# Kernel optimization log

Hardware: AMD Instinct MI355X
Metric: run time of the kernel (lower is better)

The kernel has to match this reference:

```python
import math
import jax, jax.numpy as jnp
import numpy as np

CT = {"SDD": 1000.0, "SCD": 500.0, "det_interval": 1.0, "num_det": 736}


def ramp_filter_np(ct, scale):
    # Standard equiangular fan-beam ramp filter (utility.ramp_filter):
    #   h[0] = 1/(8*db^2); h[n odd] = -1/(2*(pi*sin(n*db))^2); h[n even!=0] = 0
    db = ct["det_interval"] / ct["SDD"] * scale  # angular detector pitch at this scale
    n_det = int(ct["num_det"] // scale)
    n = np.arange(-(n_det - 1), n_det)  # length K = 2*n_det - 1
    h = np.zeros(n.shape, dtype=np.float32)
    h[n == 0] = 1.0 / (8.0 * db ** 2)
    odd = (n % 2) != 0
    h[odd] = -0.5 / (np.pi * np.sin(n[odd] * db)) ** 2
    return h


def setup_inputs() -> dict:
    key = jax.random.key(0)
    scale = 1
    batch, ch, view, det = 16, 1, 1152, CT["num_det"] // scale
    sinogram = jax.random.normal(key, (batch, ch, view, det), dtype=jnp.float32)
    delta_b = CT["det_interval"] / CT["SDD"]
    # recon_filter = ramp_filter * scale * delta_b, shaped [1,1,1,K] (OIHW)
    filt = ramp_filter_np(CT, scale) * scale * delta_b
    recon_filter = jnp.asarray(filt, dtype=jnp.float32)[None, None, None, :]
    return {"sinogram": sinogram, "recon_filter": recon_filter, "scale": scale}


def reference(sinogram, recon_filter, scale):
    det = sinogram.shape[-1]
    # cosine fan-beam pre-weighting
    s_range = (CT["det_interval"]
               * jnp.linspace((1.0 - det) / 2.0, (det - 1.0) / 2.0, det, dtype=jnp.float32)
               * scale) / CT["SDD"]
    cos_weight = (CT["SCD"] / 10000.0) * jnp.cos(s_range)  # [det]
    x = sinogram * cos_weight[None, None, None, :]
    # 1D ramp-filter convolution along detector axis (F.conv2d with 1xK kernel)
    K = recon_filter.shape[-1]
    pad = K // 2
    out = jax.lax.conv_general_dilated(
        x, recon_filter,
        window_strides=(1, 1),
        padding=[(0, 0), (pad, pad)],
        dimension_numbers=("NCHW", "OIHW", "NCHW"),
    )
    return out
```

## Files before the change

kernel.cpp:

```cpp
#include <hip/hip_runtime.h>
#include <stdint.h>

typedef unsigned short ushort_t;
typedef ushort_t u16x8 __attribute__((ext_vector_type(8)));
typedef __bf16 bf16x8 __attribute__((ext_vector_type(8)));
typedef float f32x4 __attribute__((ext_vector_type(4)));

#define DET 736
#define NPAD 768

#define GPTR(p) ((const __attribute__((address_space(1))) unsigned int*)(p))
#define LPTR(p) ((__attribute__((address_space(3))) unsigned int*)(p))

__device__ __forceinline__ ushort_t f2bf(float f) {
    unsigned u = __builtin_bit_cast(unsigned, f);
    u += 0x7FFFu + ((u >> 16) & 1u);
    return (ushort_t)(u >> 16);
}

__global__ void cast_x(const float* __restrict__ in, ushort_t* __restrict__ out, int total) {
    int idx = (blockIdx.x * blockDim.x + threadIdx.x) * 8;
    if (idx >= total) return;
    float4 a = *(const float4*)(in + idx);
    float4 b = *(const float4*)(in + idx + 4);
    u16x8 o;
    o[0] = f2bf(a.x); o[1] = f2bf(a.y); o[2] = f2bf(a.z); o[3] = f2bf(a.w);
    o[4] = f2bf(b.x); o[5] = f2bf(b.y); o[6] = f2bf(b.z); o[7] = f2bf(b.w);
    *(u16x8*)(out + idx) = o;
}

__global__ void prep_bt(const float* __restrict__ filt, ushort_t* __restrict__ Bt) {
    int idx = blockIdx.x * blockDim.x + threadIdx.x;
    if (idx >= NPAD * DET) return;
    int n = idx / DET;
    int k = idx - n * DET;
    float w = 0.05f * cosf(((float)k - 367.5f) * 0.001f);
    float v = (n < DET) ? w * filt[k - n + (DET - 1)] : 0.0f;
    Bt[idx] = f2bf(v);
}

__global__ __launch_bounds__(256) void gemm_bt(
    const ushort_t* __restrict__ A,
    const ushort_t* __restrict__ Bt,
    float* __restrict__ C, int M)
{
    __shared__ ushort_t As[128 * 32];
    __shared__ ushort_t Bs[128 * 32];

    const int tid  = threadIdx.x;
    const int lane = tid & 63;
    const int warp = tid >> 6;
    const int wm   = warp & 1;
    const int wn   = warp >> 1;
    const int quad = lane >> 4;
    const int l16  = lane & 15;

    const size_t row_a0 = (size_t)blockIdx.x * 128;
    const size_t row_b0 = (size_t)blockIdx.y * 128;

    const int c0 = warp * 64 + lane;
    const int c1 = c0 + 256;
    const int r0 = c0 >> 2, q0 = c0 & 3;
    const int r1 = c1 >> 2, q1 = c1 & 3;

    const ushort_t* a0p = A  + (row_a0 + r0) * DET + q0 * 8;
    const ushort_t* a1p = A  + (row_a0 + r1) * DET + q1 * 8;
    const ushort_t* b0p = Bt + (row_b0 + r0) * DET + q0 * 8;
    const ushort_t* b1p = Bt + (row_b0 + r1) * DET + q1 * 8;

    f32x4 acc[4][4];
#pragma unroll
    for (int i = 0; i < 4; ++i)
#pragma unroll
        for (int jx = 0; jx < 4; ++jx)
            acc[i][jx] = (f32x4){0.f, 0.f, 0.f, 0.f};

    for (int k0 = 0; k0 < DET; k0 += 32) {
        if (k0) __syncthreads();
        __builtin_amdgcn_global_load_lds(GPTR(a0p + k0), LPTR(As + warp * 512),        16, 0, 0);
        __builtin_amdgcn_global_load_lds(GPTR(a1p + k0), LPTR(As + 2048 + warp * 512), 16, 0, 0);
        __builtin_amdgcn_global_load_lds(GPTR(b0p + k0), LPTR(Bs + warp * 512),        16, 0, 0);
        __builtin_amdgcn_global_load_lds(GPTR(b1p + k0), LPTR(Bs + 2048 + warp * 512), 16, 0, 0);
        __syncthreads();

        u16x8 af[4], bfr[4];
#pragma unroll
        for (int mi = 0; mi < 4; ++mi)
            af[mi] = *(const u16x8*)(As + (wm * 64 + mi * 16 + l16) * 32 + quad * 8);
#pragma unroll
        for (int ni = 0; ni < 4; ++ni)
            bfr[ni] = *(const u16x8*)(Bs + (wn * 64 + ni * 16 + l16) * 32 + quad * 8);
#pragma unroll
        for (int mi = 0; mi < 4; ++mi)
#pragma unroll
            for (int ni = 0; ni < 4; ++ni)
                acc[mi][ni] = __builtin_amdgcn_mfma_f32_16x16x32_bf16(
                    __builtin_bit_cast(bf16x8, af[mi]),
                    __builtin_bit_cast(bf16x8, bfr[ni]),
                    acc[mi][ni], 0, 0, 0);
    }

#pragma unroll
    for (int mi = 0; mi < 4; ++mi) {
#pragma unroll
        for (int ni = 0; ni < 4; ++ni) {
            int colg = (int)row_b0 + wn * 64 + ni * 16 + l16;
            if (colg < DET) {
#pragma unroll
                for (int r = 0; r < 4; ++r) {
                    size_t rowg = row_a0 + wm * 64 + mi * 16 + quad * 4 + r;
                    C[rowg * DET + colg] = acc[mi][ni][r];
                }
            }
        }
    }
}

extern "C" void kernel_launch(void* const* d_in, const int* in_sizes, int n_in,
                              void* d_out, int out_size, void* d_ws, size_t ws_size,
                              hipStream_t stream) {
    const float* sino = (const float*)d_in[0];
    const float* filt = (const float*)d_in[1];
    int total = in_sizes[0];
    int M = total / DET;

    ushort_t* Xbf = (ushort_t*)d_ws;
    ushort_t* Btb = Xbf + (size_t)total;
    float* out = (float*)d_out;

    cast_x<<<(total / 8 + 255) / 256, 256, 0, stream>>>(sino, Xbf, total);
    prep_bt<<<(NPAD * DET + 255) / 256, 256, 0, stream>>>(filt, Btb);

    dim3 grid(M / 128, NPAD / 128);
    gemm_bt<<<grid, 256, 0, stream>>>(Xbf, Btb, out, M);
}
```

Measured before the change: 144.0 us.

## Fuse fp32-to-bf16 cast into GEMM with register-prefetched double-buffered LDS

Removes the separate cast kernel and its bf16 intermediate buffer. The GEMM now reads fp32 sinogram rows directly and converts them to bf16 in registers before storing to LDS. The main loop is double-buffered: the next K tile is loaded into registers while MFMAs run on the current tile, and LDS rows are padded to stride 40 to reduce bank conflicts. In exchange, the A tile is read from global memory as fp32 by every N-block, which doubles A read bytes per block. It also gives up the direct global-to-LDS load path and uses more registers.

New measurement: 148.9 us. 1.03x slower.

```diff
diff --git a/kernel.cpp b/kernel.cpp
--- a/kernel.cpp
+++ b/kernel.cpp
@@ -1,5 +1,4 @@
 #include <hip/hip_runtime.h>
-#include <stdint.h>
 
 typedef unsigned short ushort_t;
 typedef ushort_t u16x8 __attribute__((ext_vector_type(8)));
@@ -8,25 +7,13 @@
 
 #define DET 736
 #define NPAD 768
-
-#define GPTR(p) ((const __attribute__((address_space(1))) unsigned int*)(p))
-#define LPTR(p) ((__attribute__((address_space(3))) unsigned int*)(p))
+#define NITER 23
+#define LDSTR 40
 
 __device__ __forceinline__ ushort_t f2bf(float f) {
     unsigned u = __builtin_bit_cast(unsigned, f);
     u += 0x7FFFu + ((u >> 16) & 1u);
     return (ushort_t)(u >> 16);
-}
-
-__global__ void cast_x(const float* __restrict__ in, ushort_t* __restrict__ out, int total) {
-    int idx = (blockIdx.x * blockDim.x + threadIdx.x) * 8;
-    if (idx >= total) return;
-    float4 a = *(const float4*)(in + idx);
-    float4 b = *(const float4*)(in + idx + 4);
-    u16x8 o;
-    o[0] = f2bf(a.x); o[1] = f2bf(a.y); o[2] = f2bf(a.z); o[3] = f2bf(a.w);
-    o[4] = f2bf(b.x); o[5] = f2bf(b.y); o[6] = f2bf(b.z); o[7] = f2bf(b.w);
-    *(u16x8*)(out + idx) = o;
 }
 
 __global__ void prep_bt(const float* __restrict__ filt, ushort_t* __restrict__ Bt) {
@@ -39,13 +26,13 @@
     Bt[idx] = f2bf(v);
 }
 
-__global__ __launch_bounds__(256) void gemm_bt(
-    const ushort_t* __restrict__ A,
+__global__ __launch_bounds__(256) void gemm_fused(
+    const float* __restrict__ A,
     const ushort_t* __restrict__ Bt,
     float* __restrict__ C, int M)
 {
-    __shared__ ushort_t As[128 * 32];
-    __shared__ ushort_t Bs[128 * 32];
+    __shared__ ushort_t As[2][128 * LDSTR];
+    __shared__ ushort_t Bs[2][128 * LDSTR];
 
     const int tid  = threadIdx.x;
     const int lane = tid & 63;
@@ -58,15 +45,11 @@
     const size_t row_a0 = (size_t)blockIdx.x * 128;
     const size_t row_b0 = (size_t)blockIdx.y * 128;
 
-    const int c0 = warp * 64 + lane;
-    const int c1 = c0 + 256;
-    const int r0 = c0 >> 2, q0 = c0 & 3;
-    const int r1 = c1 >> 2, q1 = c1 & 3;
-
-    const ushort_t* a0p = A  + (row_a0 + r0) * DET + q0 * 8;
-    const ushort_t* a1p = A  + (row_a0 + r1) * DET + q1 * 8;
-    const ushort_t* b0p = Bt + (row_b0 + r0) * DET + q0 * 8;
-    const ushort_t* b1p = Bt + (row_b0 + r1) * DET + q1 * 8;
+    const int srow = tid >> 1;
+    const int sh   = (tid & 1) * 16;
+    const float*    ap = A  + (row_a0 + srow) * DET + sh;
+    const ushort_t* bp = Bt + (row_b0 + srow) * DET + sh;
+    const int soff = srow * LDSTR + sh;
 
     f32x4 acc[4][4];
 #pragma unroll
@@ -75,21 +58,48 @@
         for (int jx = 0; jx < 4; ++jx)
             acc[i][jx] = (f32x4){0.f, 0.f, 0.f, 0.f};
 
-    for (int k0 = 0; k0 < DET; k0 += 32) {
-        if (k0) __syncthreads();
-        __builtin_amdgcn_global_load_lds(GPTR(a0p + k0), LPTR(As + warp * 512),        16, 0, 0);
-        __builtin_amdgcn_global_load_lds(GPTR(a1p + k0), LPTR(As + 2048 + warp * 512), 16, 0, 0);
-        __builtin_amdgcn_global_load_lds(GPTR(b0p + k0), LPTR(Bs + warp * 512),        16, 0, 0);
-        __builtin_amdgcn_global_load_lds(GPTR(b1p + k0), LPTR(Bs + 2048 + warp * 512), 16, 0, 0);
-        __syncthreads();
+    {
+        f32x4 a0 = *(const f32x4*)(ap + 0);
+        f32x4 a1 = *(const f32x4*)(ap + 4);
+        f32x4 a2 = *(const f32x4*)(ap + 8);
+        f32x4 a3 = *(const f32x4*)(ap + 12);
+        u16x8 b0 = *(const u16x8*)(bp + 0);
+        u16x8 b1 = *(const u16x8*)(bp + 8);
+        bf16x8 c0 = {(__bf16)a0[0], (__bf16)a0[1], (__bf16)a0[2], (__bf16)a0[3],
+                     (__bf16)a1[0], (__bf16)a1[1], (__bf16)a1[2], (__bf16)a1[3]};
+        bf16x8 c1 = {(__bf16)a2[0], (__bf16)a2[1], (__bf16)a2[2], (__bf16)a2[3],
+                     (__bf16)a3[0], (__bf16)a3[1], (__bf16)a3[2], (__bf16)a3[3]};
+        *(u16x8*)(&As[0][soff])     = __builtin_bit_cast(u16x8, c0);
+        *(u16x8*)(&As[0][soff + 8]) = __builtin_bit_cast(u16x8, c1);
+        *(u16x8*)(&Bs[0][soff])     = b0;
+        *(u16x8*)(&Bs[0][soff + 8]) = b1;
+    }
+    __syncthreads();
+
+    for (int it = 0; it < NITER; ++it) {
+        const int cur = it & 1;
+        const int nxt = cur ^ 1;
+        const int k1 = (it + 1) * 32;
+        const bool pf = (it + 1 < NITER);
+
+        f32x4 a0, a1, a2, a3; u16x8 b0, b1;
+        if (pf) {
+            a0 = *(const f32x4*)(ap + k1);
+            a1 = *(const f32x4*)(ap + k1 + 4);
+            a2 = *(const f32x4*)(ap + k1 + 8);
+            a3 = *(const f32x4*)(ap + k1 + 12);
+            b0 = *(const u16x8*)(bp + k1);
+            b1 = *(const u16x8*)(bp + k1 + 8);
+        }
 
         u16x8 af[4], bfr[4];
 #pragma unroll
         for (int mi = 0; mi < 4; ++mi)
-            af[mi] = *(const u16x8*)(As + (wm * 64 + mi * 16 + l16) * 32 + quad * 8);
+            af[mi] = *(const u16x8*)(&As[cur][(wm * 64 + mi * 16 + l16) * LDSTR + quad * 8]);
 #pragma unroll
         for (int ni = 0; ni < 4; ++ni)
-            bfr[ni] = *(const u16x8*)(Bs + (wn * 64 + ni * 16 + l16) * 32 + quad * 8);
+            bfr[ni] = *(const u16x8*)(&Bs[cur][(wn * 64 + ni * 16 + l16) * LDSTR + quad * 8]);
+
 #pragma unroll
         for (int mi = 0; mi < 4; ++mi)
 #pragma unroll
@@ -98,6 +108,18 @@
                     __builtin_bit_cast(bf16x8, af[mi]),
                     __builtin_bit_cast(bf16x8, bfr[ni]),
                     acc[mi][ni], 0, 0, 0);
+
+        if (pf) {
+            bf16x8 c0 = {(__bf16)a0[0], (__bf16)a0[1], (__bf16)a0[2], (__bf16)a0[3],
+                         (__bf16)a1[0], (__bf16)a1[1], (__bf16)a1[2], (__bf16)a1[3]};
+            bf16x8 c1 = {(__bf16)a2[0], (__bf16)a2[1], (__bf16)a2[2], (__bf16)a2[3],
+                         (__bf16)a3[0], (__bf16)a3[1], (__bf16)a3[2], (__bf16)a3[3]};
+            *(u16x8*)(&As[nxt][soff])     = __builtin_bit_cast(u16x8, c0);
+            *(u16x8*)(&As[nxt][soff + 8]) = __builtin_bit_cast(u16x8, c1);
+            *(u16x8*)(&Bs[nxt][soff])     = b0;
+            *(u16x8*)(&Bs[nxt][soff + 8]) = b1;
+        }
+        __syncthreads();
     }
 
 #pragma unroll
@@ -124,13 +146,11 @@
     int total = in_sizes[0];
     int M = total / DET;
 
-    ushort_t* Xbf = (ushort_t*)d_ws;
-    ushort_t* Btb = Xbf + (size_t)total;
+    ushort_t* Btb = (ushort_t*)d_ws;
     float* out = (float*)d_out;
 
-    cast_x<<<(total / 8 + 255) / 256, 256, 0, stream>>>(sino, Xbf, total);
-    prep_bt<<<(NPAD * DET + 255) / 256, 256, 0, stream>>>(filt, Btb);
+    prep_bt<<<(NPAD * DET) / 256, 256, 0, stream>>>(filt, Btb);
 
     dim3 grid(M / 128, NPAD / 128);
-    gemm_bt<<<grid, 256, 0, stream>>>(Xbf, Btb, out, M);
+    gemm_fused<<<grid, 256, 0, stream>>>(sino, Btb, out, M);
 }
```

## Shrink GEMM N-tile to 64 and load tiles via registers with prefetch

Applied to the files above, without the earlier changes.

Cuts the N tile of the filter-as-GEMM kernel from 128 to 64, which halves the B shared-memory buffer and the accumulator count and doubles the grid along N. Replaces the direct global-to-LDS loads with vector loads into registers, issued before the barrier so they overlap the previous iteration's MFMA work, then stores them to LDS. Adds a launch-bounds occupancy hint. The intent is more resident blocks and better latency hiding, at the cost of more A-tile re-reads from global memory and an extra register round trip.

Result: no change. 145.1 us (+0.7%).

```diff
diff --git a/kernel.cpp b/kernel.cpp
--- a/kernel.cpp
+++ b/kernel.cpp
@@ -1,5 +1,4 @@
 #include <hip/hip_runtime.h>
-#include <stdint.h>
 
 typedef unsigned short ushort_t;
 typedef ushort_t u16x8 __attribute__((ext_vector_type(8)));
@@ -8,9 +7,7 @@
 
 #define DET 736
 #define NPAD 768
-
-#define GPTR(p) ((const __attribute__((address_space(1))) unsigned int*)(p))
-#define LPTR(p) ((__attribute__((address_space(3))) unsigned int*)(p))
+#define NITER 23
 
 __device__ __forceinline__ ushort_t f2bf(float f) {
     unsigned u = __builtin_bit_cast(unsigned, f);
@@ -39,13 +36,13 @@
     Bt[idx] = f2bf(v);
 }
 
-__global__ __launch_bounds__(256) void gemm_bt(
+__global__ __launch_bounds__(256, 6) void gemm_bt(
     const ushort_t* __restrict__ A,
     const ushort_t* __restrict__ Bt,
     float* __restrict__ C, int M)
 {
     __shared__ ushort_t As[128 * 32];
-    __shared__ ushort_t Bs[128 * 32];
+    __shared__ ushort_t Bs[64 * 32];
 
     const int tid  = threadIdx.x;
     const int lane = tid & 63;
@@ -56,44 +53,46 @@
     const int l16  = lane & 15;
 
     const size_t row_a0 = (size_t)blockIdx.x * 128;
-    const size_t row_b0 = (size_t)blockIdx.y * 128;
+    const size_t row_b0 = (size_t)blockIdx.y * 64;
 
-    const int c0 = warp * 64 + lane;
-    const int c1 = c0 + 256;
-    const int r0 = c0 >> 2, q0 = c0 & 3;
-    const int r1 = c1 >> 2, q1 = c1 & 3;
+    const int ca0 = tid, ca1 = tid + 256;
+    const int ra0 = ca0 >> 2, qa0 = ca0 & 3;
+    const int ra1 = ca1 >> 2, qa1 = ca1 & 3;
+    const int rb  = tid >> 2, qb  = tid & 3;
 
-    const ushort_t* a0p = A  + (row_a0 + r0) * DET + q0 * 8;
-    const ushort_t* a1p = A  + (row_a0 + r1) * DET + q1 * 8;
-    const ushort_t* b0p = Bt + (row_b0 + r0) * DET + q0 * 8;
-    const ushort_t* b1p = Bt + (row_b0 + r1) * DET + q1 * 8;
+    const ushort_t* a0p = A  + (row_a0 + ra0) * DET + qa0 * 8;
+    const ushort_t* a1p = A  + (row_a0 + ra1) * DET + qa1 * 8;
+    const ushort_t* b0p = Bt + (row_b0 + rb)  * DET + qb  * 8;
 
-    f32x4 acc[4][4];
+    f32x4 acc[4][2];
 #pragma unroll
     for (int i = 0; i < 4; ++i)
 #pragma unroll
-        for (int jx = 0; jx < 4; ++jx)
+        for (int jx = 0; jx < 2; ++jx)
             acc[i][jx] = (f32x4){0.f, 0.f, 0.f, 0.f};
 
-    for (int k0 = 0; k0 < DET; k0 += 32) {
-        if (k0) __syncthreads();
-        __builtin_amdgcn_global_load_lds(GPTR(a0p + k0), LPTR(As + warp * 512),        16, 0, 0);
-        __builtin_amdgcn_global_load_lds(GPTR(a1p + k0), LPTR(As + 2048 + warp * 512), 16, 0, 0);
-        __builtin_amdgcn_global_load_lds(GPTR(b0p + k0), LPTR(Bs + warp * 512),        16, 0, 0);
-        __builtin_amdgcn_global_load_lds(GPTR(b1p + k0), LPTR(Bs + 2048 + warp * 512), 16, 0, 0);
+    for (int it = 0; it < NITER; ++it) {
+        const int k0 = it * 32;
+        u16x8 a0 = *(const u16x8*)(a0p + k0);
+        u16x8 a1 = *(const u16x8*)(a1p + k0);
+        u16x8 b0 = *(const u16x8*)(b0p + k0);
+        if (it) __syncthreads();
+        *(u16x8*)(As + ca0 * 8) = a0;
+        *(u16x8*)(As + ca1 * 8) = a1;
+        *(u16x8*)(Bs + tid * 8) = b0;
         __syncthreads();
 
-        u16x8 af[4], bfr[4];
+        u16x8 af[4], bfr[2];
 #pragma unroll
         for (int mi = 0; mi < 4; ++mi)
             af[mi] = *(const u16x8*)(As + (wm * 64 + mi * 16 + l16) * 32 + quad * 8);
 #pragma unroll
-        for (int ni = 0; ni < 4; ++ni)
-            bfr[ni] = *(const u16x8*)(Bs + (wn * 64 + ni * 16 + l16) * 32 + quad * 8);
+        for (int ni = 0; ni < 2; ++ni)
+            bfr[ni] = *(const u16x8*)(Bs + (wn * 32 + ni * 16 + l16) * 32 + quad * 8);
 #pragma unroll
         for (int mi = 0; mi < 4; ++mi)
 #pragma unroll
-            for (int ni = 0; ni < 4; ++ni)
+            for (int ni = 0; ni < 2; ++ni)
                 acc[mi][ni] = __builtin_amdgcn_mfma_f32_16x16x32_bf16(
                     __builtin_bit_cast(bf16x8, af[mi]),
                     __builtin_bit_cast(bf16x8, bfr[ni]),
@@ -103,8 +102,8 @@
 #pragma unroll
     for (int mi = 0; mi < 4; ++mi) {
 #pragma unroll
-        for (int ni = 0; ni < 4; ++ni) {
-            int colg = (int)row_b0 + wn * 64 + ni * 16 + l16;
+        for (int ni = 0; ni < 2; ++ni) {
+            int colg = (int)row_b0 + wn * 32 + ni * 16 + l16;
             if (colg < DET) {
 #pragma unroll
                 for (int r = 0; r < 4; ++r) {
@@ -129,8 +128,8 @@
     float* out = (float*)d_out;
 
     cast_x<<<(total / 8 + 255) / 256, 256, 0, stream>>>(sino, Xbf, total);
-    prep_bt<<<(NPAD * DET + 255) / 256, 256, 0, stream>>>(filt, Btb);
+    prep_bt<<<(NPAD * DET) / 256, 256, 0, stream>>>(filt, Btb);
 
-    dim3 grid(M / 128, NPAD / 128);
+    dim3 grid(M / 128, NPAD / 64);
     gemm_bt<<<grid, 256, 0, stream>>>(Xbf, Btb, out, M);
 }
```

## Pre-swizzle A and B into MFMA fragment order and stage B fully in LDS

Applied to the files above, without the earlier changes.

The cast and filter-prep kernels now write A and B in a fragment-major swizzled layout matching the MFMA 16x16x32 operand order. The GEMM reads A fragments directly from global memory with coalesced 16-byte loads and skips LDS for A. All of B's 64-column K panel goes into LDS in two halves, which cuts the barriers per K step. The tile changes to 256x64 per block with launch_bounds occupancy 3. This trades B reuse across A rows, since each warp now loads its own A rows, for fewer synchronisations. The grid and M are hardcoded to 18432 rows.

After: 144.0 us. About the same (-0.0%).

```diff
diff --git a/kernel.cpp b/kernel.cpp
--- a/kernel.cpp
+++ b/kernel.cpp
@@ -1,5 +1,4 @@
 #include <hip/hip_runtime.h>
-#include <stdint.h>
 
 typedef unsigned short ushort_t;
 typedef ushort_t u16x8 __attribute__((ext_vector_type(8)));
@@ -8,9 +7,8 @@
 
 #define DET 736
 #define NPAD 768
-
-#define GPTR(p) ((const __attribute__((address_space(1))) unsigned int*)(p))
-#define LPTR(p) ((__attribute__((address_space(3))) unsigned int*)(p))
+#define NKB 23
+#define NBY 12
 
 __device__ __forceinline__ ushort_t f2bf(float f) {
     unsigned u = __builtin_bit_cast(unsigned, f);
@@ -18,102 +16,115 @@
     return (ushort_t)(u >> 16);
 }
 
-__global__ void cast_x(const float* __restrict__ in, ushort_t* __restrict__ out, int total) {
-    int idx = (blockIdx.x * blockDim.x + threadIdx.x) * 8;
-    if (idx >= total) return;
-    float4 a = *(const float4*)(in + idx);
-    float4 b = *(const float4*)(in + idx + 4);
+__global__ void cast_swz_a(const float* __restrict__ in, ushort_t* __restrict__ out) {
+    int t = blockIdx.x * 256 + threadIdx.x;
+    int l  = t & 63;
+    int fi = t >> 6;
+    int kb = fi % NKB;
+    int rs = fi / NKB;
+    int row = rs * 16 + (l & 15);
+    int k0  = kb * 32 + (l >> 4) * 8;
+    const float* p = in + row * DET + k0;
+    float4 a = *(const float4*)p;
+    float4 b = *(const float4*)(p + 4);
     u16x8 o;
     o[0] = f2bf(a.x); o[1] = f2bf(a.y); o[2] = f2bf(a.z); o[3] = f2bf(a.w);
     o[4] = f2bf(b.x); o[5] = f2bf(b.y); o[6] = f2bf(b.z); o[7] = f2bf(b.w);
-    *(u16x8*)(out + idx) = o;
+    *(u16x8*)(out + (size_t)t * 8) = o;
 }
 
-__global__ void prep_bt(const float* __restrict__ filt, ushort_t* __restrict__ Bt) {
-    int idx = blockIdx.x * blockDim.x + threadIdx.x;
-    if (idx >= NPAD * DET) return;
-    int n = idx / DET;
-    int k = idx - n * DET;
-    float w = 0.05f * cosf(((float)k - 367.5f) * 0.001f);
-    float v = (n < DET) ? w * filt[k - n + (DET - 1)] : 0.0f;
-    Bt[idx] = f2bf(v);
+__global__ void prep_bt_swz(const float* __restrict__ filt, ushort_t* __restrict__ B) {
+    int G = blockIdx.x * 256 + threadIdx.x;
+    int l  = G & 63;
+    int ns = (G >> 6) & 3;
+    int kb = (G >> 8) % NKB;
+    int by = (G >> 8) / NKB;
+    int col = by * 64 + ns * 16 + (l & 15);
+    int k0  = kb * 32 + (l >> 4) * 8;
+    u16x8 o;
+#pragma unroll
+    for (int j = 0; j < 8; ++j) {
+        int k = k0 + j;
+        float w = 0.05f * cosf(((float)k - 367.5f) * 0.001f);
+        float v = (col < DET) ? w * filt[k - col + (DET - 1)] : 0.0f;
+        o[j] = f2bf(v);
+    }
+    *(u16x8*)(B + (size_t)G * 8) = o;
 }
 
-__global__ __launch_bounds__(256) void gemm_bt(
+__global__ __launch_bounds__(256, 3) void gemm_nb(
     const ushort_t* __restrict__ A,
-    const ushort_t* __restrict__ Bt,
-    float* __restrict__ C, int M)
+    const ushort_t* __restrict__ B,
+    float* __restrict__ C)
 {
-    __shared__ ushort_t As[128 * 32];
-    __shared__ ushort_t Bs[128 * 32];
+    __shared__ ushort_t Bs[12 * 256 * 8];
 
     const int tid  = threadIdx.x;
     const int lane = tid & 63;
-    const int warp = tid >> 6;
-    const int wm   = warp & 1;
-    const int wn   = warp >> 1;
+    const int w    = tid >> 6;
     const int quad = lane >> 4;
     const int l16  = lane & 15;
+    const int bx = blockIdx.x, by = blockIdx.y;
 
-    const size_t row_a0 = (size_t)blockIdx.x * 128;
-    const size_t row_b0 = (size_t)blockIdx.y * 128;
-
-    const int c0 = warp * 64 + lane;
-    const int c1 = c0 + 256;
-    const int r0 = c0 >> 2, q0 = c0 & 3;
-    const int r1 = c1 >> 2, q1 = c1 & 3;
-
-    const ushort_t* a0p = A  + (row_a0 + r0) * DET + q0 * 8;
-    const ushort_t* a1p = A  + (row_a0 + r1) * DET + q1 * 8;
-    const ushort_t* b0p = Bt + (row_b0 + r0) * DET + q0 * 8;
-    const ushort_t* b1p = Bt + (row_b0 + r1) * DET + q1 * 8;
+    const ushort_t* pA = A + ((size_t)(bx * 16 + w * 4) * NKB * 64 + lane) * 8;
+    const ushort_t* pB = B + (size_t)by * (NKB * 256) * 8;
 
     f32x4 acc[4][4];
 #pragma unroll
     for (int i = 0; i < 4; ++i)
 #pragma unroll
-        for (int jx = 0; jx < 4; ++jx)
-            acc[i][jx] = (f32x4){0.f, 0.f, 0.f, 0.f};
+        for (int j = 0; j < 4; ++j)
+            acc[i][j] = (f32x4){0.f, 0.f, 0.f, 0.f};
 
-    for (int k0 = 0; k0 < DET; k0 += 32) {
-        if (k0) __syncthreads();
-        __builtin_amdgcn_global_load_lds(GPTR(a0p + k0), LPTR(As + warp * 512),        16, 0, 0);
-        __builtin_amdgcn_global_load_lds(GPTR(a1p + k0), LPTR(As + 2048 + warp * 512), 16, 0, 0);
-        __builtin_amdgcn_global_load_lds(GPTR(b0p + k0), LPTR(Bs + warp * 512),        16, 0, 0);
-        __builtin_amdgcn_global_load_lds(GPTR(b1p + k0), LPTR(Bs + 2048 + warp * 512), 16, 0, 0);
-        __syncthreads();
+#define STAGE(CHUNKS, OFF)                                            \
+    for (int c = tid; c < (CHUNKS); c += 256)                         \
+        *(u16x8*)(Bs + (size_t)c * 8) = *(const u16x8*)(pB + ((size_t)(OFF) + c) * 8);
 
-        u16x8 af[4], bfr[4];
+#define BODY(KB, KB0)                                                          \
+    {                                                                          \
+        u16x8 af[4], bf[4];                                                    \
+        _Pragma("unroll")                                                      \
+        for (int mi = 0; mi < 4; ++mi)                                         \
+            af[mi] = *(const u16x8*)(pA + ((size_t)mi * NKB * 64 + (KB) * 64) * 8); \
+        _Pragma("unroll")                                                      \
+        for (int ni = 0; ni < 4; ++ni)                                         \
+            bf[ni] = *(const u16x8*)(Bs + (((KB) - (KB0)) * 256 + ni * 64 + lane) * 8); \
+        _Pragma("unroll")                                                      \
+        for (int mi = 0; mi < 4; ++mi)                                         \
+            _Pragma("unroll")                                                  \
+            for (int ni = 0; ni < 4; ++ni)                                     \
+                acc[mi][ni] = __builtin_amdgcn_mfma_f32_16x16x32_bf16(         \
+                    __builtin_bit_cast(bf16x8, af[mi]),                        \
+                    __builtin_bit_cast(bf16x8, bf[ni]),                        \
+                    acc[mi][ni], 0, 0, 0);                                     \
+    }
+
+    STAGE(12 * 256, 0)
+    __syncthreads();
 #pragma unroll
-        for (int mi = 0; mi < 4; ++mi)
-            af[mi] = *(const u16x8*)(As + (wm * 64 + mi * 16 + l16) * 32 + quad * 8);
+    for (int kb = 0; kb < 12; ++kb) BODY(kb, 0)
+    __syncthreads();
+    STAGE(11 * 256, 12 * 256)
+    __syncthreads();
 #pragma unroll
-        for (int ni = 0; ni < 4; ++ni)
-            bfr[ni] = *(const u16x8*)(Bs + (wn * 64 + ni * 16 + l16) * 32 + quad * 8);
-#pragma unroll
-        for (int mi = 0; mi < 4; ++mi)
-#pragma unroll
-            for (int ni = 0; ni < 4; ++ni)
-                acc[mi][ni] = __builtin_amdgcn_mfma_f32_16x16x32_bf16(
-                    __builtin_bit_cast(bf16x8, af[mi]),
-                    __builtin_bit_cast(bf16x8, bfr[ni]),
-                    acc[mi][ni], 0, 0, 0);
-    }
+    for (int kb = 12; kb < 23; ++kb) BODY(kb, 12)
 
 #pragma unroll
     for (int mi = 0; mi < 4; ++mi) {
 #pragma unroll
         for (int ni = 0; ni < 4; ++ni) {
-            int colg = (int)row_b0 + wn * 64 + ni * 16 + l16;
+            int colg = by * 64 + ni * 16 + l16;
             if (colg < DET) {
 #pragma unroll
                 for (int r = 0; r < 4; ++r) {
-                    size_t rowg = row_a0 + wm * 64 + mi * 16 + quad * 4 + r;
+                    size_t rowg = (size_t)bx * 256 + w * 64 + mi * 16 + quad * 4 + r;
                     C[rowg * DET + colg] = acc[mi][ni][r];
                 }
             }
         }
     }
+#undef STAGE
+#undef BODY
 }
 
 extern "C" void kernel_launch(void* const* d_in, const int* in_sizes, int n_in,
@@ -122,15 +133,14 @@
     const float* sino = (const float*)d_in[0];
     const float* filt = (const float*)d_in[1];
     int total = in_sizes[0];
-    int M = total / DET;
 
-    ushort_t* Xbf = (ushort_t*)d_ws;
-    ushort_t* Btb = Xbf + (size_t)total;
+    ushort_t* Aswz = (ushort_t*)d_ws;
+    ushort_t* Bswz = Aswz + (size_t)total;
     float* out = (float*)d_out;
 
-    cast_x<<<(total / 8 + 255) / 256, 256, 0, stream>>>(sino, Xbf, total);
-    prep_bt<<<(NPAD * DET + 255) / 256, 256, 0, stream>>>(filt, Btb);
+    cast_swz_a<<<total / 8 / 256, 256, 0, stream>>>(sino, Aswz);
+    prep_bt_swz<<<(NBY * NKB * 4 * 64) / 256, 256, 0, stream>>>(filt, Bswz);
 
-    dim3 grid(M / 128, NPAD / 128);
-    gemm_bt<<<grid, 256, 0, stream>>>(Xbf, Btb, out, M);
+    dim3 grid(18432 / 256, NBY);
+    gemm_nb<<<grid, 256, 0, stream>>>(Aswz, Bswz, out);
 }
```
